# Optimization experiments

Measured on AMD Instinct MI355X. Metric: run time of the kernel, lower is better.

The kernel has to match this reference:

```python
import jax, jax.numpy as jnp
import numpy as np

TEMPERATURE = 0.07
MASK_VAL = -65504.0  # torch code's fill value (fp16 min), note: applied BEFORE temperature division
EPS = 1e-8


def setup_inputs() -> dict:
    key = jax.random.key(0)
    z = jax.random.normal(key, (8192, 1024), dtype=jnp.float32)
    return {"z": z}


def reference(z):
    N = z.shape[0]
    # cosine similarity via normalized GEMM (torch clamps norm at eps)
    norms = jnp.maximum(jnp.linalg.norm(z, axis=-1, keepdims=True), EPS)
    zn = z / norms
    cos_sim = zn @ zn.T  # [N, N]
    eye = jnp.eye(N, dtype=bool)
    cos_sim = jnp.where(eye, MASK_VAL, cos_sim) / TEMPERATURE
    # pos_mask = eye rolled by N//2 along dim 0 -> pos_mask[i, (i - N//2) % N] = True
    idx = jnp.arange(N)
    pos = cos_sim[idx, (idx - N // 2) % N]
    nll = -pos + jax.nn.logsumexp(cos_sim, axis=-1)
    return nll.mean()
```

## Files before the change

kernel.cpp:

```cpp
#include <hip/hip_runtime.h>
#include <hip/hip_bf16.h>


#define N 8192
#define D 1024
#define INV_T 14.285714285714286f
#define NTILES 528
#define ACC_SCALE (INV_T / 1024.0f)

typedef float f32x4 __attribute__((ext_vector_type(4)));
typedef long lx2 __attribute__((ext_vector_type(2)));

__device__ inline void gload16(const void* g, void* l) {
  __builtin_amdgcn_global_load_lds(
      (const __attribute__((address_space(1))) void*)g,
      (__attribute__((address_space(3))) void*)l, 16, 0, 0);
}

__global__ __launch_bounds__(256) void k_normalize(const float* __restrict__ z,
                                                   unsigned char* __restrict__ zn8,
                                                   float* __restrict__ rowsum) {
  const int row = blockIdx.x;
  const int t = threadIdx.x;
  if (row < 32) rowsum[row * 256 + t] = 0.0f;
  const float4 v = ((const float4*)(z + (size_t)row * D))[t];
  float ss = v.x * v.x + v.y * v.y + v.z * v.z + v.w * v.w;
#pragma unroll
  for (int off = 32; off > 0; off >>= 1) ss += __shfl_down(ss, off, 64);
  __shared__ float red[4];
  __shared__ float s_inv;
  if ((t & 63) == 0) red[t >> 6] = ss;
  __syncthreads();
  if (t == 0) {
    float tot = red[0] + red[1] + red[2] + red[3];
    s_inv = 1.0f / fmaxf(sqrtf(tot), 1e-8f);
  }
  __syncthreads();
  const float sc = s_inv * 32.0f;
  int p = __builtin_amdgcn_cvt_pk_fp8_f32(v.x * sc, v.y * sc, 0, false);
  p = __builtin_amdgcn_cvt_pk_fp8_f32(v.z * sc, v.w * sc, p, true);
  ((int*)(zn8 + (size_t)row * D))[t] = p;
}

__global__ __launch_bounds__(512, 2) void k_tile(const unsigned char* __restrict__ zn8,
                                                 float* __restrict__ rowsum,
                                                 float* __restrict__ pos) {
  extern __shared__ __align__(16) char smem[];
  const int tid = threadIdx.x;
  const int w = tid >> 6, l = tid & 63;

  const int b = blockIdx.x;
  int tr = (int)((sqrtf(8.0f * (float)b + 1.0f) - 1.0f) * 0.5f);
  if (tr * (tr + 1) / 2 > b) --tr;
  if ((tr + 1) * (tr + 2) / 2 <= b) ++tr;
  const int tc = b - tr * (tr + 1) / 2;
  const bool diag = (tr == tc);

  const int wr = w >> 1, wc = w & 1;
  const int m = l & 15, kg = l >> 4;
  const int rowA0 = tr * 256, colB0 = tc * 256;

  f32x4 acc[4][8] = {};

  int srow[4], scol[4];
#pragma unroll
  for (int j = 0; j < 4; ++j) {
    int s = j * 512 + tid;
    int r = s >> 3;
    srow[j] = r;
    scol[j] = (s & 7) ^ (r & 7);
  }

  const int csw0 = (kg ^ (m & 7)) * 16;
  const int csw1 = ((kg + 4) ^ (m & 7)) * 16;

  {
    char* ab = smem;
    char* bb = smem + 32768;
#pragma unroll
    for (int j = 0; j < 4; ++j) {
      const int s = j * 512 + tid;
      gload16((const char*)zn8 + ((size_t)(rowA0 + srow[j]) * D + scol[j] * 16), ab + s * 16);
    }
    if (!diag) {
#pragma unroll
      for (int j = 0; j < 4; ++j) {
        const int s = j * 512 + tid;
        gload16((const char*)zn8 + ((size_t)(colB0 + srow[j]) * D + scol[j] * 16), bb + s * 16);
      }
    }
  }
  __syncthreads();

  for (int kt = 0; kt < 8; ++kt) {
    if (kt < 7) {
      const size_t kb = (size_t)(kt + 1) * 128;
      char* ab = smem + ((kt + 1) & 1) * 65536;
#pragma unroll
      for (int j = 0; j < 4; ++j) {
        const int s = j * 512 + tid;
        gload16((const char*)zn8 + ((size_t)(rowA0 + srow[j]) * D + kb + scol[j] * 16), ab + s * 16);
      }
      if (!diag) {
        char* bb = ab + 32768;
#pragma unroll
        for (int j = 0; j < 4; ++j) {
          const int s = j * 512 + tid;
          gload16((const char*)zn8 + ((size_t)(colB0 + srow[j]) * D + kb + scol[j] * 16), bb + s * 16);
        }
      }
    }
    const char* ab = smem + (kt & 1) * 65536;
    const char* bb = diag ? ab : (ab + 32768);

    lx2 a0[4], a1[4];
#pragma unroll
    for (int mt = 0; mt < 4; ++mt) {
      const char* rp = ab + (wr * 64 + mt * 16 + m) * 128;
      a0[mt] = *(const lx2*)(rp + csw0);
      a1[mt] = *(const lx2*)(rp + csw1);
    }
#pragma unroll
    for (int nt = 0; nt < 8; ++nt) {
      const char* rp = bb + (wc * 128 + nt * 16 + m) * 128;
      const lx2 b0 = *(const lx2*)(rp + csw0);
      const lx2 b1 = *(const lx2*)(rp + csw1);
#pragma unroll
      for (int mt = 0; mt < 4; ++mt) {
        acc[mt][nt] = __builtin_amdgcn_mfma_f32_16x16x32_fp8_fp8(a0[mt].x, b0.x, acc[mt][nt], 0, 0, 0);
        acc[mt][nt] = __builtin_amdgcn_mfma_f32_16x16x32_fp8_fp8(a0[mt].y, b0.y, acc[mt][nt], 0, 0, 0);
        acc[mt][nt] = __builtin_amdgcn_mfma_f32_16x16x32_fp8_fp8(a1[mt].x, b1.x, acc[mt][nt], 0, 0, 0);
        acc[mt][nt] = __builtin_amdgcn_mfma_f32_16x16x32_fp8_fp8(a1[mt].y, b1.y, acc[mt][nt], 0, 0, 0);
      }
    }
    __syncthreads();
  }

  const int quad = l >> 4;
  const int col = l & 15;
  float cs[8] = {0.f, 0.f, 0.f, 0.f, 0.f, 0.f, 0.f, 0.f};
#pragma unroll
  for (int mt = 0; mt < 4; ++mt) {
    float rs[4] = {0.f, 0.f, 0.f, 0.f};
#pragma unroll
    for (int nt = 0; nt < 8; ++nt) {
      const int gcol = colB0 + wc * 128 + nt * 16 + col;
#pragma unroll
      for (int r = 0; r < 4; ++r) {
        const int grow = rowA0 + wr * 64 + mt * 16 + quad * 4 + r;
        const float t = acc[mt][nt][r] * ACC_SCALE;
        if (gcol == (grow ^ (N / 2))) {
          pos[grow] = t;
          pos[gcol] = t;
        }
        const float e = (gcol == grow) ? 0.0f : __expf(t - INV_T);
        rs[r] += e;
        cs[nt] += e;
      }
    }
#pragma unroll
    for (int off = 1; off < 16; off <<= 1) {
#pragma unroll
      for (int r = 0; r < 4; ++r) rs[r] += __shfl_xor(rs[r], off, 64);
    }
    if (col == 0) {
#pragma unroll
      for (int r = 0; r < 4; ++r)
        atomicAdd(&rowsum[rowA0 + wr * 64 + mt * 16 + quad * 4 + r], rs[r]);
    }
  }
  if (!diag) {
#pragma unroll
    for (int nt = 0; nt < 8; ++nt) {
      cs[nt] += __shfl_xor(cs[nt], 16, 64);
      cs[nt] += __shfl_xor(cs[nt], 32, 64);
    }
    if (l < 16) {
#pragma unroll
      for (int nt = 0; nt < 8; ++nt)
        atomicAdd(&rowsum[colB0 + wc * 128 + nt * 16 + l], cs[nt]);
    }
  }
}

__global__ __launch_bounds__(1024) void k_final(const float* __restrict__ rowsum,
                                                const float* __restrict__ pos,
                                                float* __restrict__ out) {
  const int t = threadIdx.x;
  float s = 0.f;
  for (int i = t; i < N; i += 1024) s += INV_T + __logf(rowsum[i]) - pos[i];
#pragma unroll
  for (int off = 32; off > 0; off >>= 1) s += __shfl_down(s, off, 64);
  __shared__ float red[16];
  if ((t & 63) == 0) red[t >> 6] = s;
  __syncthreads();
  if (t == 0) {
    float tot = 0.f;
#pragma unroll
    for (int j = 0; j < 16; ++j) tot += red[j];
    out[0] = tot * (1.0f / N);
  }
}

extern "C" void kernel_launch(void* const* d_in, const int* in_sizes, int n_in,
                              void* d_out, int out_size, void* d_ws, size_t ws_size,
                              hipStream_t stream) {
  const float* z = (const float*)d_in[0];
  float* out = (float*)d_out;
  char* ws = (char*)d_ws;
  unsigned char* zn8 = (unsigned char*)ws;
  float* rowsum = (float*)(ws + (size_t)N * D);
  float* pos = (float*)(ws + (size_t)N * D + (size_t)N * 4);

  static bool attr_set = false;
  if (!attr_set) {
    hipFuncSetAttribute((const void*)k_tile,
                        hipFuncAttributeMaxDynamicSharedMemorySize, 131072);
    attr_set = true;
  }

  k_normalize<<<N, 256, 0, stream>>>(z, zn8, rowsum);
  k_tile<<<NTILES, 512, 131072, stream>>>(zn8, rowsum, pos);
  k_final<<<1, 1024, 0, stream>>>(rowsum, pos, out);
}
```

Baseline: 146.6 us.

## Single-buffer k_tile LDS for higher occupancy; normalize one row per wavefront

The GEMM tile kernel drops its 128KB double-buffered LDS pipeline for a single 64KB buffer, loaded and synchronized at each k-step. Its launch bound is raised to request 4 blocks per CU, so more tiles can be resident at once. The cost is that global-to-LDS loads no longer overlap with MFMA work. Requesting 4 blocks of 512 threads also caps each thread's registers, which may force the 128-float accumulator to spill. Separately, the normalize kernel now handles four rows per block, one per wavefront, using only shuffle reductions with no shared memory or barriers.

New measurement: 465.7 us. 218% more time.

```diff
diff --git a/kernel.cpp b/kernel.cpp
--- a/kernel.cpp
+++ b/kernel.cpp
@@ -20,29 +20,31 @@
 __global__ __launch_bounds__(256) void k_normalize(const float* __restrict__ z,
                                                    unsigned char* __restrict__ zn8,
                                                    float* __restrict__ rowsum) {
-  const int row = blockIdx.x;
   const int t = threadIdx.x;
-  if (row < 32) rowsum[row * 256 + t] = 0.0f;
-  const float4 v = ((const float4*)(z + (size_t)row * D))[t];
-  float ss = v.x * v.x + v.y * v.y + v.z * v.z + v.w * v.w;
-#pragma unroll
-  for (int off = 32; off > 0; off >>= 1) ss += __shfl_down(ss, off, 64);
-  __shared__ float red[4];
-  __shared__ float s_inv;
-  if ((t & 63) == 0) red[t >> 6] = ss;
-  __syncthreads();
-  if (t == 0) {
-    float tot = red[0] + red[1] + red[2] + red[3];
-    s_inv = 1.0f / fmaxf(sqrtf(tot), 1e-8f);
-  }
-  __syncthreads();
-  const float sc = s_inv * 32.0f;
-  int p = __builtin_amdgcn_cvt_pk_fp8_f32(v.x * sc, v.y * sc, 0, false);
-  p = __builtin_amdgcn_cvt_pk_fp8_f32(v.z * sc, v.w * sc, p, true);
-  ((int*)(zn8 + (size_t)row * D))[t] = p;
-}
-
-__global__ __launch_bounds__(512, 2) void k_tile(const unsigned char* __restrict__ zn8,
+  const int l = t & 63, w = t >> 6;
+  const int row = blockIdx.x * 4 + w;
+  if (blockIdx.x < 32) rowsum[blockIdx.x * 256 + t] = 0.0f;
+  const float4* zr = (const float4*)(z + (size_t)row * D);
+  float4 v[4];
+  float ss = 0.f;
+#pragma unroll
+  for (int j = 0; j < 4; ++j) {
+    v[j] = zr[l + 64 * j];
+    ss += v[j].x * v[j].x + v[j].y * v[j].y + v[j].z * v[j].z + v[j].w * v[j].w;
+  }
+#pragma unroll
+  for (int off = 32; off > 0; off >>= 1) ss += __shfl_xor(ss, off, 64);
+  const float sc = 32.0f / fmaxf(sqrtf(ss), 1e-8f);
+  int* op = (int*)(zn8 + (size_t)row * D);
+#pragma unroll
+  for (int j = 0; j < 4; ++j) {
+    int p = __builtin_amdgcn_cvt_pk_fp8_f32(v[j].x * sc, v[j].y * sc, 0, false);
+    p = __builtin_amdgcn_cvt_pk_fp8_f32(v[j].z * sc, v[j].w * sc, p, true);
+    op[l + 64 * j] = p;
+  }
+}
+
+__global__ __launch_bounds__(512, 4) void k_tile(const unsigned char* __restrict__ zn8,
                                                  float* __restrict__ rowsum,
                                                  float* __restrict__ pos) {
   extern __shared__ __align__(16) char smem[];
@@ -74,35 +76,17 @@
   const int csw0 = (kg ^ (m & 7)) * 16;
   const int csw1 = ((kg + 4) ^ (m & 7)) * 16;
 
-  {
-    char* ab = smem;
-    char* bb = smem + 32768;
-#pragma unroll
-    for (int j = 0; j < 4; ++j) {
-      const int s = j * 512 + tid;
-      gload16((const char*)zn8 + ((size_t)(rowA0 + srow[j]) * D + scol[j] * 16), ab + s * 16);
-    }
-    if (!diag) {
-#pragma unroll
-      for (int j = 0; j < 4; ++j) {
-        const int s = j * 512 + tid;
-        gload16((const char*)zn8 + ((size_t)(colB0 + srow[j]) * D + scol[j] * 16), bb + s * 16);
-      }
-    }
-  }
-  __syncthreads();
-
   for (int kt = 0; kt < 8; ++kt) {
-    if (kt < 7) {
-      const size_t kb = (size_t)(kt + 1) * 128;
-      char* ab = smem + ((kt + 1) & 1) * 65536;
+    const size_t kb = (size_t)kt * 128;
+    {
+      char* ab = smem;
 #pragma unroll
       for (int j = 0; j < 4; ++j) {
         const int s = j * 512 + tid;
         gload16((const char*)zn8 + ((size_t)(rowA0 + srow[j]) * D + kb + scol[j] * 16), ab + s * 16);
       }
       if (!diag) {
-        char* bb = ab + 32768;
+        char* bb = smem + 32768;
 #pragma unroll
         for (int j = 0; j < 4; ++j) {
           const int s = j * 512 + tid;
@@ -110,9 +94,10 @@
         }
       }
     }
-    const char* ab = smem + (kt & 1) * 65536;
+    __syncthreads();
+
+    const char* ab = smem;
     const char* bb = diag ? ab : (ab + 32768);
-
     lx2 a0[4], a1[4];
 #pragma unroll
     for (int mt = 0; mt < 4; ++mt) {
@@ -212,14 +197,7 @@
   float* rowsum = (float*)(ws + (size_t)N * D);
   float* pos = (float*)(ws + (size_t)N * D + (size_t)N * 4);
 
-  static bool attr_set = false;
-  if (!attr_set) {
-    hipFuncSetAttribute((const void*)k_tile,
-                        hipFuncAttributeMaxDynamicSharedMemorySize, 131072);
-    attr_set = true;
-  }
-
-  k_normalize<<<N, 256, 0, stream>>>(z, zn8, rowsum);
-  k_tile<<<NTILES, 512, 131072, stream>>>(zn8, rowsum, pos);
+  k_normalize<<<N / 4, 256, 0, stream>>>(z, zn8, rowsum);
+  k_tile<<<NTILES, 512, 65536, stream>>>(zn8, rowsum, pos);
   k_final<<<1, 1024, 0, stream>>>(rowsum, pos, out);
 }
```
